# Kernel optimization log

Measured on AMD Instinct MI355X. Metric: run time of the kernel, lower is better.

The kernel has to match this reference:

```python
import jax, jax.numpy as jnp
import numpy as np

NHEAD = 16

def setup_inputs() -> dict:
    key = jax.random.key(0)
    ks = jax.random.split(key, 7)
    b, l, d = 4, 2048, 1024
    s = 1.0 / np.sqrt(d)
    return {
        "Q": jax.random.normal(ks[0], (b, l, d), jnp.float32),
        "K": jax.random.normal(ks[1], (b, l, d), jnp.float32),
        "V": jax.random.normal(ks[2], (b, l, d), jnp.float32),
        "WQ": jax.random.normal(ks[3], (d, d), jnp.float32) * s,
        "WK": jax.random.normal(ks[4], (d, d), jnp.float32) * s,
        "WV": jax.random.normal(ks[5], (d, d), jnp.float32) * s,
        "WO": jax.random.normal(ks[6], (d, d), jnp.float32) * s,
    }

def reference(Q, K, V, WQ, WK, WV, WO):
    # WQ/WK/WV/WO stored torch-style as [out, in]; Linear(x) = x @ W.T
    b, lq, d = Q.shape
    lk = K.shape[1]
    h = NHEAD
    dk = d // h
    # project and split heads: [b, l, h, dk]
    q = (Q @ WQ.T).reshape(b, lq, h, dk)
    k = (K @ WK.T).reshape(b, lk, h, dk)
    v = (V @ WV.T).reshape(b, lk, h, dk)
    # scaled dot-product attention (dropout = identity in eval mode)
    scale = 1.0 / jnp.sqrt(jnp.asarray(dk, Q.dtype))
    score = jnp.einsum('bqhd,bkhd->bhqk', q, k) * scale  # [b,h,lq,lk]
    attn = jax.nn.softmax(score, axis=-1)
    o = jnp.einsum('bhqk,bkhd->bqhd', attn, v).reshape(b, lq, h * dk)
    return o @ WO.T
```

## Files before the change

### kernel.cpp

```cpp
#include <hip/hip_runtime.h>
#include <stdint.h>

#define D_MODEL 1024
#define NHEADS 16
#define DKH 64
#define SEQ 2048
#define BATCH 4
#define M_TOT (BATCH * SEQ)
#define LOG2E 1.44269504088896340736f

typedef __bf16 v8bf __attribute__((ext_vector_type(8)));
typedef __bf16 v4bf __attribute__((ext_vector_type(4)));
typedef _Float16 v8h __attribute__((ext_vector_type(8)));
typedef _Float16 v4h __attribute__((ext_vector_type(4)));
typedef float v4f __attribute__((ext_vector_type(4)));
typedef float v16f __attribute__((ext_vector_type(16)));
typedef unsigned int v4u __attribute__((ext_vector_type(4)));
typedef unsigned int v2u __attribute__((ext_vector_type(2)));

typedef const __attribute__((address_space(1))) void* gas_ptr;
typedef __attribute__((address_space(3))) void* las_ptr;

static __device__ __forceinline__ void async16(const void* g, void* l) {
    __builtin_amdgcn_global_load_lds((gas_ptr)g, (las_ptr)l, 16, 0, 0);
}

static __device__ __forceinline__ v4f mfma16x32(v8bf a, v8bf b, v4f c) {
    return __builtin_amdgcn_mfma_f32_16x16x32_bf16(a, b, c, 0, 0, 0);
}
static __device__ __forceinline__ v16f mfma32x16bf(v8bf a, v8bf b, v16f c) {
    return __builtin_amdgcn_mfma_f32_32x32x16_bf16(a, b, c, 0, 0, 0);
}
static __device__ __forceinline__ v16f mfma32x16h(v8h a, v8h b, v16f c) {
    return __builtin_amdgcn_mfma_f32_32x32x16_f16(a, b, c, 0, 0, 0);
}
static __device__ __forceinline__ unsigned pkh(float a, float b) {
    return __builtin_bit_cast(unsigned, __builtin_amdgcn_cvt_pkrtz(a, b));
}
static __device__ __forceinline__ void plswap(unsigned& x, unsigned& y) {
    v2u r = __builtin_amdgcn_permlane32_swap(x, y, false, false);
    x = r[0];
    y = r[1];
}
static __device__ __forceinline__ float fexp2(float x) {
#if __has_builtin(__builtin_amdgcn_exp2f)
    return __builtin_amdgcn_exp2f(x);
#else
    float r;
    asm("v_exp_f32 %0, %1" : "=v"(r) : "v"(x));
    return r;
#endif
}

__global__ __launch_bounds__(256) void cvt_x(const float* __restrict__ src,
                                             __bf16* __restrict__ dst) {
    int i = blockIdx.x * 256 + threadIdx.x;
    const float4* s = (const float4*)src;
    float4 a = s[2 * i], b = s[2 * i + 1];
    v8bf o;
    o[0] = (__bf16)a.x; o[1] = (__bf16)a.y; o[2] = (__bf16)a.z; o[3] = (__bf16)a.w;
    o[4] = (__bf16)b.x; o[5] = (__bf16)b.y; o[6] = (__bf16)b.z; o[7] = (__bf16)b.w;
    *(v8bf*)(dst + (size_t)i * 8) = o;
}

__global__ __launch_bounds__(256) void cvt_w(const float* __restrict__ w0,
                                             const float* __restrict__ w1,
                                             const float* __restrict__ w2,
                                             const float* __restrict__ w3,
                                             __bf16* __restrict__ dst) {
    int gid = blockIdx.x * 256 + threadIdx.x;
    int tsel = gid >> 17;
    int off = gid & 131071;
    const float* s = (tsel == 0) ? w0 : (tsel == 1) ? w1 : (tsel == 2) ? w2 : w3;
    const float4* sp = (const float4*)s + 2 * (size_t)off;
    float4 a = sp[0], b = sp[1];
    v8bf o;
    o[0] = (__bf16)a.x; o[1] = (__bf16)a.y; o[2] = (__bf16)a.z; o[3] = (__bf16)a.w;
    o[4] = (__bf16)b.x; o[5] = (__bf16)b.y; o[6] = (__bf16)b.z; o[7] = (__bf16)b.w;
    *(v8bf*)(dst + ((size_t)tsel << 20) + (size_t)off * 8) = o;
}

template <int LAYOUT>
__global__ __launch_bounds__(256) void gemm_nt(const __bf16* __restrict__ A,
                                               const __bf16* __restrict__ W,
                                               void* __restrict__ Cv, float scale) {
    const int t = threadIdx.x, lane = t & 63, wave = t >> 6;
    const int r = lane & 15, qd = lane >> 4;
    const int m0 = blockIdx.x * 128, n0 = blockIdx.y * 128;
    const int mw = (wave & 1) * 64, nw = (wave >> 1) * 64;

    __shared__ __align__(16) __bf16 As[128 * 32];
    __shared__ __align__(16) __bf16 Bs[128 * 32];

    const int wc = (lane & 3) ^ ((lane >> 3) & 3);
    const int wrow = lane >> 2;
    const int rdpos = (qd ^ ((r >> 1) & 3)) * 8;

    v4f acc[4][4] = {};
    for (int k0 = 0; k0 < D_MODEL; k0 += 32) {
#pragma unroll
        for (int p = 0; p < 2; ++p) {
            int rb = (p * 4 + wave) * 16;
            async16(A + (size_t)(m0 + rb + wrow) * D_MODEL + k0 + wc * 8, &As[rb * 32]);
            async16(W + (size_t)(n0 + rb + wrow) * D_MODEL + k0 + wc * 8, &Bs[rb * 32]);
        }
        __syncthreads();
        v8bf af[4], bfr[4];
#pragma unroll
        for (int mt = 0; mt < 4; ++mt)
            af[mt] = *(const v8bf*)&As[(mw + mt * 16 + r) * 32 + rdpos];
#pragma unroll
        for (int nt = 0; nt < 4; ++nt)
            bfr[nt] = *(const v8bf*)&Bs[(nw + nt * 16 + r) * 32 + rdpos];
#pragma unroll
        for (int mt = 0; mt < 4; ++mt)
#pragma unroll
            for (int nt = 0; nt < 4; ++nt)
                acc[mt][nt] = mfma16x32(af[mt], bfr[nt], acc[mt][nt]);
        __syncthreads();
    }

#pragma unroll
    for (int mt = 0; mt < 4; ++mt)
#pragma unroll
        for (int nt = 0; nt < 4; ++nt) {
            int row = m0 + mw + mt * 16 + qd * 4;
            int col = n0 + nw + nt * 16 + r;
            if (LAYOUT == 0) {
                float* C = (float*)Cv;
#pragma unroll
                for (int i = 0; i < 4; ++i)
                    C[(size_t)(row + i) * D_MODEL + col] = acc[mt][nt][i];
            } else {
                int bb = row >> 11, l = row & (SEQ - 1);
                int h = col >> 6, d = col & (DKH - 1);
                if (LAYOUT == 2) {
                    _Float16* vt = (_Float16*)Cv;
                    v4h o;
#pragma unroll
                    for (int i = 0; i < 4; ++i) o[i] = (_Float16)acc[mt][nt][i];
                    *(v4h*)&vt[((size_t)((bb * NHEADS + h) * DKH + d)) * SEQ + l] = o;
                } else {
                    __bf16* dst = (__bf16*)Cv;
#pragma unroll
                    for (int i = 0; i < 4; ++i)
                        dst[(((size_t)(bb * NHEADS + h) * SEQ) + l + i) * DKH + d] =
                            (__bf16)(acc[mt][nt][i] * scale);
                }
            }
        }
}

__global__ __launch_bounds__(256, 2) void attn_kernel(const __bf16* __restrict__ qh,
                                                      const __bf16* __restrict__ kh,
                                                      const _Float16* __restrict__ vt,
                                                      __bf16* __restrict__ oh) {
    const int lane = threadIdx.x & 63, wave = threadIdx.x >> 6;
    const int l31 = lane & 31, hi = lane >> 5, l7 = lane & 7;
    const int id = blockIdx.x;
    const int bh = (id & 7) * 8 + ((id >> 3) & 7);
    const int q0 = (id >> 6) * 256 + wave * 64;

    __shared__ __align__(16) __bf16 Kb[2][64 * 64];
    __shared__ __align__(16) _Float16 Vb[2][64 * 64];

    const __bf16* kbh = kh + (size_t)bh * SEQ * DKH;
    const _Float16* vbh = vt + (size_t)bh * DKH * SEQ;

    v8bf qf[2][4];
#pragma unroll
    for (int qa = 0; qa < 2; ++qa)
#pragma unroll
        for (int c = 0; c < 4; ++c)
            qf[qa][c] = *(const v8bf*)&qh[((size_t)bh * SEQ + q0 + qa * 32 + l31) * DKH +
                                          c * 16 + hi * 8];

    v16f oacc[2][2] = {};
    float ps[2] = {0.f, 0.f};
    const v16f dz = {};

    const int srow = lane >> 3;
    const int sc = (lane & 7) ^ srow;

#pragma unroll
    for (int p = 0; p < 2; ++p) {
        int rb = wave * 16 + p * 8;
        async16(kbh + (size_t)(rb + srow) * DKH + sc * 8, &Kb[0][rb * 64]);
        async16(vbh + (size_t)(rb + srow) * SEQ + sc * 8, &Vb[0][rb * 64]);
    }

    for (int tt = 0; tt < SEQ / 64; ++tt) {
        const int buf = tt & 1;
        __syncthreads();
        if (tt + 1 < SEQ / 64) {
            const int t0 = (tt + 1) * 64;
#pragma unroll
            for (int p = 0; p < 2; ++p) {
                int rb = wave * 16 + p * 8;
                async16(kbh + (size_t)(t0 + rb + srow) * DKH + sc * 8, &Kb[buf ^ 1][rb * 64]);
                async16(vbh + (size_t)(rb + srow) * SEQ + t0 + sc * 8, &Vb[buf ^ 1][rb * 64]);
            }
        }
        const __bf16* Kc = Kb[buf];
        const _Float16* Vc = Vb[buf];
#pragma unroll
        for (int kb = 0; kb < 2; ++kb) {
            v8bf ka[4];
#pragma unroll
            for (int c = 0; c < 4; ++c)
                ka[c] = *(const v8bf*)&Kc[(kb * 32 + l31) * 64 + (((c * 2 + hi) ^ l7) << 3)];
            v8h pb[2][2];
#pragma unroll
            for (int qa = 0; qa < 2; ++qa) {
                v16f d = mfma32x16bf(ka[0], qf[qa][0], dz);
#pragma unroll
                for (int c = 1; c < 4; ++c) d = mfma32x16bf(ka[c], qf[qa][c], d);
                float e[16];
#pragma unroll
                for (int i = 0; i < 16; ++i) e[i] = fexp2(d[i]);
                ps[qa] += (((e[0] + e[1]) + (e[2] + e[3])) + ((e[4] + e[5]) + (e[6] + e[7]))) +
                          (((e[8] + e[9]) + (e[10] + e[11])) + ((e[12] + e[13]) + (e[14] + e[15])));
#pragma unroll
                for (int kc = 0; kc < 2; ++kc) {
                    unsigned a0 = pkh(e[kc * 8 + 0], e[kc * 8 + 1]);
                    unsigned a1 = pkh(e[kc * 8 + 2], e[kc * 8 + 3]);
                    unsigned b0 = pkh(e[kc * 8 + 4], e[kc * 8 + 5]);
                    unsigned b1 = pkh(e[kc * 8 + 6], e[kc * 8 + 7]);
                    plswap(a0, b0);
                    plswap(a1, b1);
                    v4u w = {a0, a1, b0, b1};
                    pb[qa][kc] = __builtin_bit_cast(v8h, w);
                }
            }
#pragma unroll
            for (int dg = 0; dg < 2; ++dg)
#pragma unroll
                for (int kc = 0; kc < 2; ++kc) {
                    v8h va = *(const v8h*)&Vc[(dg * 32 + l31) * 64 +
                                              (((kb * 4 + kc * 2 + hi) ^ l7) << 3)];
#pragma unroll
                    for (int qa = 0; qa < 2; ++qa)
                        oacc[qa][dg] = mfma32x16h(va, pb[qa][kc], oacc[qa][dg]);
                }
        }
    }

    const int b = bh >> 4, h = bh & (NHEADS - 1);
#pragma unroll
    for (int qa = 0; qa < 2; ++qa) {
        float tot = ps[qa] + __shfl_xor(ps[qa], 32, 64);
        float inv = 1.0f / tot;
        int lq = q0 + qa * 32 + l31;
        __bf16* op = oh + (((size_t)(b * SEQ + lq)) * NHEADS + h) * DKH;
#pragma unroll
        for (int dg = 0; dg < 2; ++dg)
#pragma unroll
            for (int g = 0; g < 4; ++g) {
                v4bf ov;
#pragma unroll
                for (int i = 0; i < 4; ++i) ov[i] = (__bf16)(oacc[qa][dg][g * 4 + i] * inv);
                *(v4bf*)(op + dg * 32 + g * 8 + hi * 4) = ov;
            }
    }
}

extern "C" void kernel_launch(void* const* d_in, const int* in_sizes, int n_in,
                              void* d_out, int out_size, void* d_ws, size_t ws_size,
                              hipStream_t stream) {
    const float* Q = (const float*)d_in[0];
    const float* K = (const float*)d_in[1];
    const float* V = (const float*)d_in[2];
    const float* WQ = (const float*)d_in[3];
    const float* WK = (const float*)d_in[4];
    const float* WV = (const float*)d_in[5];
    const float* WO = (const float*)d_in[6];
    float* out = (float*)d_out;

    const size_t elems = (size_t)M_TOT * D_MODEL;
    const size_t welems = (size_t)D_MODEL * D_MODEL;
    __bf16* wb = (__bf16*)d_ws;
    __bf16* xb = wb + 4 * welems;
    __bf16* qh = xb + elems;
    __bf16* kh = qh + elems;
    _Float16* vtb = (_Float16*)(kh + elems);
    __bf16* oh = (__bf16*)(vtb + elems);

    dim3 gg(M_TOT / 128, D_MODEL / 128);

    cvt_w<<<2048, 256, 0, stream>>>(WQ, WK, WV, WO, wb);
    cvt_x<<<4096, 256, 0, stream>>>(Q, xb);
    gemm_nt<1><<<gg, 256, 0, stream>>>(xb, wb, qh, 0.125f * LOG2E);
    cvt_x<<<4096, 256, 0, stream>>>(K, xb);
    gemm_nt<1><<<gg, 256, 0, stream>>>(xb, wb + welems, kh, 1.0f);
    cvt_x<<<4096, 256, 0, stream>>>(V, xb);
    gemm_nt<2><<<gg, 256, 0, stream>>>(xb, wb + 2 * welems, vtb, 1.0f);
    attn_kernel<<<512, 256, 0, stream>>>(qh, kh, vtb, oh);
    gemm_nt<0><<<gg, 256, 0, stream>>>(oh, wb + 3 * welems, out, 1.0f);
}
```

Baseline: 331.2 us.

## Batch Q/K/V conversion and projection into single launches, add MFMA priority hints

Converts Q, K and V to bf16 in one launch into separate buffers, then runs the three projection GEMMs as one grid with a z dimension selecting the input, weight and output layout. This removes six serialized launches and their tail effects by giving the GPU three times as many blocks at once. It also wraps the attention MFMA sequences in s_setprio raises so matrix ops get issue priority over the exp work of other waves. The fused path needs more workspace and falls back to the old sequence when the workspace is too small.

Measured after the change: 323.6 us. -2.3%, faster.

```diff
diff --git a/kernel.cpp b/kernel.cpp
--- a/kernel.cpp
+++ b/kernel.cpp
@@ -55,6 +55,24 @@
 __global__ __launch_bounds__(256) void cvt_x(const float* __restrict__ src,
                                              __bf16* __restrict__ dst) {
     int i = blockIdx.x * 256 + threadIdx.x;
+    const float4* s = (const float4*)src;
+    float4 a = s[2 * i], b = s[2 * i + 1];
+    v8bf o;
+    o[0] = (__bf16)a.x; o[1] = (__bf16)a.y; o[2] = (__bf16)a.z; o[3] = (__bf16)a.w;
+    o[4] = (__bf16)b.x; o[5] = (__bf16)b.y; o[6] = (__bf16)b.z; o[7] = (__bf16)b.w;
+    *(v8bf*)(dst + (size_t)i * 8) = o;
+}
+
+__global__ __launch_bounds__(256) void cvt_x3(const float* __restrict__ s0,
+                                              const float* __restrict__ s1,
+                                              const float* __restrict__ s2,
+                                              __bf16* __restrict__ d0,
+                                              __bf16* __restrict__ d1,
+                                              __bf16* __restrict__ d2) {
+    int t = blockIdx.x >> 12;
+    int i = (blockIdx.x & 4095) * 256 + threadIdx.x;
+    const float* src = (t == 0) ? s0 : (t == 1) ? s1 : s2;
+    __bf16* dst = (t == 0) ? d0 : (t == 1) ? d1 : d2;
     const float4* s = (const float4*)src;
     float4 a = s[2 * i], b = s[2 * i + 1];
     v8bf o;
@@ -151,6 +169,77 @@
         }
 }
 
+__global__ __launch_bounds__(256) void gemm_qkv(const __bf16* __restrict__ xq,
+                                                const __bf16* __restrict__ xk,
+                                                const __bf16* __restrict__ xv,
+                                                const __bf16* __restrict__ wb,
+                                                __bf16* __restrict__ qh,
+                                                __bf16* __restrict__ kh,
+                                                _Float16* __restrict__ vtb, float qs) {
+    const int z = blockIdx.z;
+    const __bf16* A = (z == 0) ? xq : (z == 1) ? xk : xv;
+    const __bf16* W = wb + (size_t)z * D_MODEL * D_MODEL;
+
+    const int t = threadIdx.x, lane = t & 63, wave = t >> 6;
+    const int r = lane & 15, qd = lane >> 4;
+    const int m0 = blockIdx.x * 128, n0 = blockIdx.y * 128;
+    const int mw = (wave & 1) * 64, nw = (wave >> 1) * 64;
+
+    __shared__ __align__(16) __bf16 As[128 * 32];
+    __shared__ __align__(16) __bf16 Bs[128 * 32];
+
+    const int wc = (lane & 3) ^ ((lane >> 3) & 3);
+    const int wrow = lane >> 2;
+    const int rdpos = (qd ^ ((r >> 1) & 3)) * 8;
+
+    v4f acc[4][4] = {};
+    for (int k0 = 0; k0 < D_MODEL; k0 += 32) {
+#pragma unroll
+        for (int p = 0; p < 2; ++p) {
+            int rb = (p * 4 + wave) * 16;
+            async16(A + (size_t)(m0 + rb + wrow) * D_MODEL + k0 + wc * 8, &As[rb * 32]);
+            async16(W + (size_t)(n0 + rb + wrow) * D_MODEL + k0 + wc * 8, &Bs[rb * 32]);
+        }
+        __syncthreads();
+        v8bf af[4], bfr[4];
+#pragma unroll
+        for (int mt = 0; mt < 4; ++mt)
+            af[mt] = *(const v8bf*)&As[(mw + mt * 16 + r) * 32 + rdpos];
+#pragma unroll
+        for (int nt = 0; nt < 4; ++nt)
+            bfr[nt] = *(const v8bf*)&Bs[(nw + nt * 16 + r) * 32 + rdpos];
+#pragma unroll
+        for (int mt = 0; mt < 4; ++mt)
+#pragma unroll
+            for (int nt = 0; nt < 4; ++nt)
+                acc[mt][nt] = mfma16x32(af[mt], bfr[nt], acc[mt][nt]);
+        __syncthreads();
+    }
+
+    const float scale = (z == 0) ? qs : 1.0f;
+#pragma unroll
+    for (int mt = 0; mt < 4; ++mt)
+#pragma unroll
+        for (int nt = 0; nt < 4; ++nt) {
+            int row = m0 + mw + mt * 16 + qd * 4;
+            int col = n0 + nw + nt * 16 + r;
+            int bb = row >> 11, l = row & (SEQ - 1);
+            int h = col >> 6, d = col & (DKH - 1);
+            if (z == 2) {
+                v4h o;
+#pragma unroll
+                for (int i = 0; i < 4; ++i) o[i] = (_Float16)acc[mt][nt][i];
+                *(v4h*)&vtb[((size_t)((bb * NHEADS + h) * DKH + d)) * SEQ + l] = o;
+            } else {
+                __bf16* dst = (z == 0) ? qh : kh;
+#pragma unroll
+                for (int i = 0; i < 4; ++i)
+                    dst[(((size_t)(bb * NHEADS + h) * SEQ) + l + i) * DKH + d] =
+                        (__bf16)(acc[mt][nt][i] * scale);
+            }
+        }
+}
+
 __global__ __launch_bounds__(256, 2) void attn_kernel(const __bf16* __restrict__ qh,
                                                       const __bf16* __restrict__ kh,
                                                       const _Float16* __restrict__ vt,
@@ -212,9 +301,11 @@
             v8h pb[2][2];
 #pragma unroll
             for (int qa = 0; qa < 2; ++qa) {
+                __builtin_amdgcn_s_setprio(1);
                 v16f d = mfma32x16bf(ka[0], qf[qa][0], dz);
 #pragma unroll
                 for (int c = 1; c < 4; ++c) d = mfma32x16bf(ka[c], qf[qa][c], d);
+                __builtin_amdgcn_s_setprio(0);
                 float e[16];
 #pragma unroll
                 for (int i = 0; i < 16; ++i) e[i] = fexp2(d[i]);
@@ -232,6 +323,7 @@
                     pb[qa][kc] = __builtin_bit_cast(v8h, w);
                 }
             }
+            __builtin_amdgcn_s_setprio(1);
 #pragma unroll
             for (int dg = 0; dg < 2; ++dg)
 #pragma unroll
@@ -242,6 +334,7 @@
                     for (int qa = 0; qa < 2; ++qa)
                         oacc[qa][dg] = mfma32x16h(va, pb[qa][kc], oacc[qa][dg]);
                 }
+            __builtin_amdgcn_s_setprio(0);
         }
     }
 
@@ -278,22 +371,42 @@
 
     const size_t elems = (size_t)M_TOT * D_MODEL;
     const size_t welems = (size_t)D_MODEL * D_MODEL;
-    __bf16* wb = (__bf16*)d_ws;
-    __bf16* xb = wb + 4 * welems;
-    __bf16* qh = xb + elems;
-    __bf16* kh = qh + elems;
-    _Float16* vtb = (_Float16*)(kh + elems);
-    __bf16* oh = (__bf16*)(vtb + elems);
+    const size_t fused_need = 8 * welems + 6 * 2 * elems;
 
     dim3 gg(M_TOT / 128, D_MODEL / 128);
 
-    cvt_w<<<2048, 256, 0, stream>>>(WQ, WK, WV, WO, wb);
-    cvt_x<<<4096, 256, 0, stream>>>(Q, xb);
-    gemm_nt<1><<<gg, 256, 0, stream>>>(xb, wb, qh, 0.125f * LOG2E);
-    cvt_x<<<4096, 256, 0, stream>>>(K, xb);
-    gemm_nt<1><<<gg, 256, 0, stream>>>(xb, wb + welems, kh, 1.0f);
-    cvt_x<<<4096, 256, 0, stream>>>(V, xb);
-    gemm_nt<2><<<gg, 256, 0, stream>>>(xb, wb + 2 * welems, vtb, 1.0f);
-    attn_kernel<<<512, 256, 0, stream>>>(qh, kh, vtb, oh);
-    gemm_nt<0><<<gg, 256, 0, stream>>>(oh, wb + 3 * welems, out, 1.0f);
-}
+    if (ws_size >= fused_need) {
+        __bf16* wb = (__bf16*)d_ws;
+        __bf16* xq = wb + 4 * welems;
+        __bf16* xk = xq + elems;
+        __bf16* xv = xk + elems;
+        __bf16* qh = xv + elems;
+        __bf16* kh = qh + elems;
+        _Float16* vtb = (_Float16*)(kh + elems);
+        __bf16* oh = xq;
+
+        cvt_w<<<2048, 256, 0, stream>>>(WQ, WK, WV, WO, wb);
+        cvt_x3<<<3 * 4096, 256, 0, stream>>>(Q, K, V, xq, xk, xv);
+        dim3 gz(M_TOT / 128, D_MODEL / 128, 3);
+        gemm_qkv<<<gz, 256, 0, stream>>>(xq, xk, xv, wb, qh, kh, vtb, 0.125f * LOG2E);
+        attn_kernel<<<512, 256, 0, stream>>>(qh, kh, vtb, oh);
+        gemm_nt<0><<<gg, 256, 0, stream>>>(oh, wb + 3 * welems, out, 1.0f);
+    } else {
+        __bf16* wb = (__bf16*)d_ws;
+        __bf16* xb = wb + 4 * welems;
+        __bf16* qh = xb + elems;
+        __bf16* kh = qh + elems;
+        _Float16* vtb = (_Float16*)(kh + elems);
+        __bf16* oh = (__bf16*)(vtb + elems);
+
+        cvt_w<<<2048, 256, 0, stream>>>(WQ, WK, WV, WO, wb);
+        cvt_x<<<4096, 256, 0, stream>>>(Q, xb);
+        gemm_nt<1><<<gg, 256, 0, stream>>>(xb, wb, qh, 0.125f * LOG2E);
+        cvt_x<<<4096, 256, 0, stream>>>(K, xb);
+        gemm_nt<1><<<gg, 256, 0, stream>>>(xb, wb + welems, kh, 1.0f);
+        cvt_x<<<4096, 256, 0, stream>>>(V, xb);
+        gemm_nt<2><<<gg, 256, 0, stream>>>(xb, wb + 2 * welems, vtb, 1.0f);
+        attn_kernel<<<512, 256, 0, stream>>>(qh, kh, vtb, oh);
+        gemm_nt<0><<<gg, 256, 0, stream>>>(oh, wb + 3 * welems, out, 1.0f);
+    }
+}
```
